# Kernel optimization log

Measured on AMD Instinct MI355X. Metric: run time of the kernel, lower is better.

The kernel has to match this reference:

```python
import jax, jax.numpy as jnp
import numpy as np

NUM_HEADS = 16
SPAN = 256  # pos_ebd_size (position_buckets)


def _split_heads(x, num_heads):
    # x: (B, S, D) -> (B*num_heads, S, D//num_heads)
    b, s, d = x.shape
    return x.reshape(b, s, num_heads, d // num_heads).transpose(0, 2, 1, 3).reshape(b * num_heads, s, d // num_heads)


def setup_inputs() -> dict:
    key = jax.random.key(0)
    ks = jax.random.split(key, 12)
    B, S, D = 1, 2048, 1024
    std = 0.02
    n_src = NUM_HEADS * S * 2 * SPAN   # flat size of c2p/p2c score tensor
    n_dst = NUM_HEADS * S * S          # flat size of gathered bias
    return {
        "hidden_states": jax.random.normal(ks[0], (B, S, D), jnp.float32),
        "rel_embeddings": jax.random.normal(ks[1], (2 * SPAN, D), jnp.float32),
        "Wq": jax.random.normal(ks[2], (D, D), jnp.float32) * std,
        "bq": jnp.zeros((D,), jnp.float32),
        "Wk": jax.random.normal(ks[3], (D, D), jnp.float32) * std,
        "bk": jnp.zeros((D,), jnp.float32),
        "Wv": jax.random.normal(ks[4], (D, D), jnp.float32) * std,
        "bv": jnp.zeros((D,), jnp.float32),
        "ids": jax.random.randint(ks[5], (n_dst,), 0, n_src, jnp.int32),
        "ids_t": jax.random.randint(ks[6], (n_dst,), 0, n_src, jnp.int32),
    }


def reference(hidden_states, rel_embeddings, Wq, bq, Wk, bk, Wv, bv, ids, ids_t):
    B, S, D = hidden_states.shape
    dh = D // NUM_HEADS
    # pos_att_type = ['c2p','p2c'] -> scale_factor = 3
    scale = jnp.sqrt(jnp.asarray(dh * 3, jnp.float32))

    q = _split_heads(hidden_states @ Wq + bq, NUM_HEADS)  # (B*H, S, dh)
    k = _split_heads(hidden_states @ Wk + bk, NUM_HEADS)
    v = _split_heads(hidden_states @ Wv + bv, NUM_HEADS)

    scores = jnp.einsum('bsd,btd->bst', q, k) / scale  # (B*H, S, S)

    # share_att_key=True: reuse key/query projections on relative embeddings
    pos = rel_embeddings[: 2 * SPAN][None]             # (1, 2*SPAN, D)
    pos_k = _split_heads(pos @ Wk + bk, NUM_HEADS)     # (H, 2*SPAN, dh)
    pos_q = _split_heads(pos @ Wq + bq, NUM_HEADS)

    bs = q.shape[0]  # == H when B == 1 (required by the original bmm)
    # c2p: gather from flattened (bs, S, 2*SPAN) scores
    c2p = jnp.einsum('bsd,bkd->bsk', q, pos_k)
    c2p_bias = c2p.reshape(-1)[ids].reshape(bs, S, S) / scale
    # p2c: gather then transpose last two dims
    p2c = jnp.einsum('bsd,bkd->bsk', k, pos_q)
    p2c_bias = jnp.swapaxes(p2c.reshape(-1)[ids_t].reshape(bs, S, S), -1, -2) / scale

    scores = scores + c2p_bias + p2c_bias
    probs = jax.nn.softmax(scores, axis=-1)
    ctx = jnp.einsum('bst,btd->bsd', probs, v)         # (B*H, S, dh)
    ctx = ctx.reshape(B, NUM_HEADS, S, dh).transpose(0, 2, 1, 3).reshape(B, S, D)
    return ctx
```

## Files before the change

kernel.cpp:

```cpp
#include <hip/hip_runtime.h>
#include <math.h>

#define S_LEN 2048
#define D_DIM 1024
#define NH 16
#define DH 64
#define NPOS 512
#define NT (S_LEN / 64)

typedef int   ivec4 __attribute__((ext_vector_type(4)));
typedef int   ivec2 __attribute__((ext_vector_type(2)));
typedef float fvec4 __attribute__((ext_vector_type(4)));

__device__ __forceinline__ void bar_lgkm() {
  asm volatile("s_waitcnt lgkmcnt(0)" ::: "memory");
  __builtin_amdgcn_s_barrier();
}

__global__ __launch_bounds__(256) void proj_gemm(
    const float* __restrict__ X, const float* __restrict__ W,
    const float* __restrict__ bias, float* __restrict__ outp, int M) {
  __shared__ float xt[16][132];
  __shared__ float wt[16][128];
  const int tid = threadIdx.x;
  const int br = blockIdx.y, bc = blockIdx.x;
  const int r0 = (tid >> 4) * 8, c0 = (tid & 15) * 8;
  float acc[8][8];
  #pragma unroll
  for (int i = 0; i < 8; i++)
    #pragma unroll
    for (int j = 0; j < 8; j++) acc[i][j] = 0.f;

  const float* Xb = X + (size_t)br * 128 * D_DIM;
  const float* Wb = W + bc * 128;

  for (int k0 = 0; k0 < D_DIM; k0 += 16) {
    __syncthreads();
    #pragma unroll
    for (int i = 0; i < 2; i++) {
      int slot = tid + i * 256;
      int row = slot >> 2;
      int kc = (slot & 3) * 4;
      float4 xv = *(const float4*)(Xb + (size_t)row * D_DIM + k0 + kc);
      xt[kc + 0][row] = xv.x; xt[kc + 1][row] = xv.y;
      xt[kc + 2][row] = xv.z; xt[kc + 3][row] = xv.w;
      int kr = slot >> 5;
      int wc = (slot & 31) * 4;
      *(float4*)&wt[kr][wc] = *(const float4*)(Wb + (size_t)(k0 + kr) * D_DIM + wc);
    }
    __syncthreads();
    #pragma unroll
    for (int kk = 0; kk < 16; kk++) {
      float a[8], b[8];
      *(float4*)&a[0] = *(const float4*)&xt[kk][r0];
      *(float4*)&a[4] = *(const float4*)&xt[kk][r0 + 4];
      *(float4*)&b[0] = *(const float4*)&wt[kk][c0];
      *(float4*)&b[4] = *(const float4*)&wt[kk][c0 + 4];
      #pragma unroll
      for (int ii = 0; ii < 8; ii++)
        #pragma unroll
        for (int jj = 0; jj < 8; jj++)
          acc[ii][jj] = fmaf(a[ii], b[jj], acc[ii][jj]);
    }
  }

  const int n0 = bc * 128 + c0;
  const int h = n0 >> 6, iw = n0 & 63;
  float bvals[8];
  #pragma unroll
  for (int jj = 0; jj < 8; jj++) bvals[jj] = bias[n0 + jj];
  #pragma unroll
  for (int ii = 0; ii < 8; ii++) {
    size_t row = (size_t)br * 128 + r0 + ii;
    float ov[8];
    #pragma unroll
    for (int jj = 0; jj < 8; jj++) ov[jj] = acc[ii][jj] + bvals[jj];
    float* dst = outp + ((size_t)h * M + row) * 64 + iw;
    *(float4*)dst = *(float4*)&ov[0];
    *(float4*)(dst + 4) = *(float4*)&ov[4];
  }
}

__global__ __launch_bounds__(256) void rel_gemm(
    const float* __restrict__ q_ws, const float* __restrict__ k_ws,
    const float* __restrict__ pk_ws, const float* __restrict__ pq_ws,
    float* __restrict__ c2p, float* __restrict__ p2c, float inv_scale) {
  __shared__ float at[16][132];
  __shared__ float bt[16][132];
  const int tid = threadIdx.x;
  const int h = blockIdx.z & 15;
  const int which = blockIdx.z >> 4;
  const float* A = (which ? k_ws : q_ws) + (size_t)h * S_LEN * DH;
  const float* Bm = (which ? pq_ws : pk_ws) + (size_t)h * NPOS * DH;
  float* C = (which ? p2c : c2p) + (size_t)h * S_LEN * NPOS;
  const int br = blockIdx.y, bc = blockIdx.x;
  const int r0 = (tid >> 4) * 8, c0 = (tid & 15) * 8;
  float acc[8][8];
  #pragma unroll
  for (int i = 0; i < 8; i++)
    #pragma unroll
    for (int j = 0; j < 8; j++) acc[i][j] = 0.f;

  for (int k0 = 0; k0 < DH; k0 += 16) {
    __syncthreads();
    #pragma unroll
    for (int i = 0; i < 2; i++) {
      int slot = tid + i * 256;
      int row = slot >> 2;
      int kc = (slot & 3) * 4;
      float4 av = *(const float4*)(A + (size_t)(br * 128 + row) * DH + k0 + kc);
      at[kc + 0][row] = av.x; at[kc + 1][row] = av.y;
      at[kc + 2][row] = av.z; at[kc + 3][row] = av.w;
      float4 bv = *(const float4*)(Bm + (size_t)(bc * 128 + row) * DH + k0 + kc);
      bt[kc + 0][row] = bv.x; bt[kc + 1][row] = bv.y;
      bt[kc + 2][row] = bv.z; bt[kc + 3][row] = bv.w;
    }
    __syncthreads();
    #pragma unroll
    for (int kk = 0; kk < 16; kk++) {
      float a[8], b[8];
      *(float4*)&a[0] = *(const float4*)&at[kk][r0];
      *(float4*)&a[4] = *(const float4*)&at[kk][r0 + 4];
      *(float4*)&b[0] = *(const float4*)&bt[kk][c0];
      *(float4*)&b[4] = *(const float4*)&bt[kk][c0 + 4];
      #pragma unroll
      for (int ii = 0; ii < 8; ii++)
        #pragma unroll
        for (int jj = 0; jj < 8; jj++)
          acc[ii][jj] = fmaf(a[ii], b[jj], acc[ii][jj]);
    }
  }
  #pragma unroll
  for (int ii = 0; ii < 8; ii++) {
    size_t row = (size_t)br * 128 + r0 + ii;
    float ov[8];
    #pragma unroll
    for (int jj = 0; jj < 8; jj++) ov[jj] = acc[ii][jj] * inv_scale;
    float* dst = C + row * NPOS + bc * 128 + c0;
    *(float4*)dst = *(float4*)&ov[0];
    *(float4*)(dst + 4) = *(float4*)&ov[4];
  }
}

__global__ __launch_bounds__(512, 4) void attn_kernel(
    const float* __restrict__ q_ws, const float* __restrict__ k_ws,
    const float* __restrict__ v_ws, const float* __restrict__ c2p,
    const float* __restrict__ p2c, const int* __restrict__ ids,
    const int* __restrict__ ids_t, float* __restrict__ outp, float inv_scale) {
  __shared__ float qT[64][68];
  __shared__ float kT[64][68];
  __shared__ float vS[64][64];
  const int tid = threadIdx.x;
  const int h = blockIdx.y;
  const int s0 = blockIdx.x * 64;
  const int r4 = tid >> 4;
  const int c4 = tid & 15;
  const int r0 = r4 * 2;
  const int c0 = c4 * 4;

  const float* qb = q_ws + ((size_t)h * S_LEN + s0) * DH;
  const float* kb = k_ws + (size_t)h * S_LEN * DH;
  const float* vb = v_ws + (size_t)h * S_LEN * DH;
  const int* idc = ids   + (size_t)h * S_LEN * S_LEN;
  const int* idp = ids_t + (size_t)h * S_LEN * S_LEN;

  #pragma unroll
  for (int i = 0; i < 2; i++) {
    int slot = tid + i * 512;
    int s = slot >> 4;
    int dc = (slot & 15) * 4;
    float4 qv = *(const float4*)(qb + (size_t)s * DH + dc);
    qT[dc + 0][s] = qv.x; qT[dc + 1][s] = qv.y;
    qT[dc + 2][s] = qv.z; qT[dc + 3][s] = qv.w;
  }

  float m[2], l[2], o[2][4];
  #pragma unroll
  for (int ii = 0; ii < 2; ii++) {
    m[ii] = -INFINITY; l[ii] = 0.f;
    #pragma unroll
    for (int jj = 0; jj < 4; jj++) o[ii][jj] = 0.f;
  }

  ivec4 ia[2];
  ivec2 ib[4];
  #pragma unroll
  for (int ii = 0; ii < 2; ii++)
    ia[ii] = __builtin_nontemporal_load(
        (const ivec4*)(idc + (size_t)(s0 + r0 + ii) * S_LEN + c0));
  #pragma unroll
  for (int jj = 0; jj < 4; jj++)
    ib[jj] = __builtin_nontemporal_load(
        (const ivec2*)(idp + (size_t)(c0 + jj) * S_LEN + s0 + r0));

  for (int kt = 0; kt < NT; kt++) {
    const int t0 = kt * 64;

    float4 kreg[2], vreg[2];
    int ts[2], dcs[2];
    #pragma unroll
    for (int i = 0; i < 2; i++) {
      int slot = tid + i * 512;
      ts[i] = slot >> 4;
      dcs[i] = (slot & 15) * 4;
      kreg[i] = *(const float4*)(kb + (size_t)(t0 + ts[i]) * DH + dcs[i]);
      vreg[i] = *(const float4*)(vb + (size_t)(t0 + ts[i]) * DH + dcs[i]);
    }

    float gc[2][4], gp[4][2];
    #pragma unroll
    for (int ii = 0; ii < 2; ii++) {
      gc[ii][0] = c2p[ia[ii][0]]; gc[ii][1] = c2p[ia[ii][1]];
      gc[ii][2] = c2p[ia[ii][2]]; gc[ii][3] = c2p[ia[ii][3]];
    }
    #pragma unroll
    for (int jj = 0; jj < 4; jj++) {
      gp[jj][0] = p2c[ib[jj][0]];
      gp[jj][1] = p2c[ib[jj][1]];
    }

    bar_lgkm();
    #pragma unroll
    for (int i = 0; i < 2; i++) {
      kT[dcs[i] + 0][ts[i]] = kreg[i].x; kT[dcs[i] + 1][ts[i]] = kreg[i].y;
      kT[dcs[i] + 2][ts[i]] = kreg[i].z; kT[dcs[i] + 3][ts[i]] = kreg[i].w;
      *(float4*)&vS[ts[i]][dcs[i]] = vreg[i];
    }
    bar_lgkm();

    float sc[2][4];
    #pragma unroll
    for (int ii = 0; ii < 2; ii++)
      #pragma unroll
      for (int jj = 0; jj < 4; jj++) sc[ii][jj] = 0.f;
    #pragma unroll 8
    for (int d = 0; d < 64; d++) {
      float a[2], b[4];
      *(float2*)a = *(const float2*)&qT[d][r0];
      *(float4*)b = *(const float4*)&kT[d][c0];
      #pragma unroll
      for (int ii = 0; ii < 2; ii++)
        #pragma unroll
        for (int jj = 0; jj < 4; jj++)
          sc[ii][jj] = fmaf(a[ii], b[jj], sc[ii][jj]);
    }

    if (kt + 1 < NT) {
      #pragma unroll
      for (int ii = 0; ii < 2; ii++)
        ia[ii] = __builtin_nontemporal_load(
            (const ivec4*)(idc + (size_t)(s0 + r0 + ii) * S_LEN + t0 + 64 + c0));
      #pragma unroll
      for (int jj = 0; jj < 4; jj++)
        ib[jj] = __builtin_nontemporal_load(
            (const ivec2*)(idp + (size_t)(t0 + 64 + c0 + jj) * S_LEN + s0 + r0));
    }

    #pragma unroll
    for (int ii = 0; ii < 2; ii++)
      #pragma unroll
      for (int jj = 0; jj < 4; jj++)
        sc[ii][jj] = fmaf(sc[ii][jj], inv_scale, gc[ii][jj] + gp[jj][ii]);

    #pragma unroll
    for (int ii = 0; ii < 2; ii++) {
      float v = fmaxf(fmaxf(sc[ii][0], sc[ii][1]), fmaxf(sc[ii][2], sc[ii][3]));
      v = fmaxf(v, __shfl_xor(v, 1));
      v = fmaxf(v, __shfl_xor(v, 2));
      v = fmaxf(v, __shfl_xor(v, 4));
      v = fmaxf(v, __shfl_xor(v, 8));
      float mn = fmaxf(m[ii], v);
      float alpha = __expf(m[ii] - mn);
      m[ii] = mn;
      float rs = 0.f;
      #pragma unroll
      for (int jj = 0; jj < 4; jj++) {
        sc[ii][jj] = __expf(sc[ii][jj] - mn);
        rs += sc[ii][jj];
      }
      rs += __shfl_xor(rs, 1);
      rs += __shfl_xor(rs, 2);
      rs += __shfl_xor(rs, 4);
      rs += __shfl_xor(rs, 8);
      l[ii] = l[ii] * alpha + rs;
      #pragma unroll
      for (int jj = 0; jj < 4; jj++) o[ii][jj] *= alpha;
    }

    bar_lgkm();
    #pragma unroll
    for (int jj = 0; jj < 4; jj++) {
      float pv[2] = {sc[0][jj], sc[1][jj]};
      *(float2*)&kT[c0 + jj][r0] = *(float2*)pv;
    }
    bar_lgkm();

    #pragma unroll 8
    for (int t = 0; t < 64; t++) {
      float a[2], b[4];
      *(float2*)a = *(const float2*)&kT[t][r0];
      *(float4*)b = *(const float4*)&vS[t][c0];
      #pragma unroll
      for (int ii = 0; ii < 2; ii++)
        #pragma unroll
        for (int jj = 0; jj < 4; jj++)
          o[ii][jj] = fmaf(a[ii], b[jj], o[ii][jj]);
    }
  }

  #pragma unroll
  for (int ii = 0; ii < 2; ii++) {
    float inv_l = 1.0f / l[ii];
    fvec4 ov;
    #pragma unroll
    for (int jj = 0; jj < 4; jj++) ov[jj] = o[ii][jj] * inv_l;
    float* dst = outp + (size_t)(s0 + r0 + ii) * D_DIM + h * DH + c0;
    __builtin_nontemporal_store(ov, (fvec4*)dst);
  }
}

extern "C" void kernel_launch(void* const* d_in, const int* in_sizes, int n_in,
                              void* d_out, int out_size, void* d_ws, size_t ws_size,
                              hipStream_t stream) {
  const float* hs  = (const float*)d_in[0];
  const float* rel = (const float*)d_in[1];
  const float* Wq  = (const float*)d_in[2];
  const float* bq  = (const float*)d_in[3];
  const float* Wk  = (const float*)d_in[4];
  const float* bk  = (const float*)d_in[5];
  const float* Wv  = (const float*)d_in[6];
  const float* bv  = (const float*)d_in[7];
  const int* ids   = (const int*)d_in[8];
  const int* ids_t = (const int*)d_in[9];
  float* outp = (float*)d_out;

  float* ws = (float*)d_ws;
  float* q_ws  = ws;
  float* k_ws  = q_ws + 2097152;
  float* v_ws  = k_ws + 2097152;
  float* pk_ws = v_ws + 2097152;
  float* pq_ws = pk_ws + 524288;
  float* c2p_ws = pq_ws + 524288;
  float* p2c_ws = c2p_ws + 16777216;

  const float inv_scale = 1.0f / sqrtf((float)(DH * 3));

  dim3 blk(256);
  proj_gemm<<<dim3(8, 16), blk, 0, stream>>>(hs, Wq, bq, q_ws, S_LEN);
  proj_gemm<<<dim3(8, 16), blk, 0, stream>>>(hs, Wk, bk, k_ws, S_LEN);
  proj_gemm<<<dim3(8, 16), blk, 0, stream>>>(hs, Wv, bv, v_ws, S_LEN);
  proj_gemm<<<dim3(8, 4),  blk, 0, stream>>>(rel, Wk, bk, pk_ws, NPOS);
  proj_gemm<<<dim3(8, 4),  blk, 0, stream>>>(rel, Wq, bq, pq_ws, NPOS);
  rel_gemm<<<dim3(4, 16, 32), blk, 0, stream>>>(q_ws, k_ws, pk_ws, pq_ws,
                                                c2p_ws, p2c_ws, inv_scale);
  attn_kernel<<<dim3(32, 16), dim3(512), 0, stream>>>(
      q_ws, k_ws, v_ws, c2p_ws, p2c_ws, ids, ids_t, outp, inv_scale);
}
```

Baseline: 3.605 ms.

## Merge five projection GEMMs into one launch with double-buffered LDS prefetch

The five separate projection GEMM launches are replaced by one kernel that selects its operands from blockIdx.z, so the small rel-embedding projections share the device with the large ones and launch overhead drops. The k-loop now uses double-buffered shared memory and issues the next tile's global loads into registers before computing on the current tile, hiding load latency. It doubles LDS use and raises register pressure, and blocks with no rows early-exit in the z=3,4 slices.

```diff
diff --git a/kernel.cpp b/kernel.cpp
--- a/kernel.cpp
+++ b/kernel.cpp
@@ -17,13 +17,29 @@
   __builtin_amdgcn_s_barrier();
 }
 
-__global__ __launch_bounds__(256) void proj_gemm(
-    const float* __restrict__ X, const float* __restrict__ W,
-    const float* __restrict__ bias, float* __restrict__ outp, int M) {
-  __shared__ float xt[16][132];
-  __shared__ float wt[16][128];
+__global__ __launch_bounds__(256) void proj_gemm5(
+    const float* __restrict__ hs, const float* __restrict__ rel,
+    const float* __restrict__ Wq, const float* __restrict__ bq,
+    const float* __restrict__ Wk, const float* __restrict__ bk,
+    const float* __restrict__ Wv, const float* __restrict__ bv,
+    float* __restrict__ q_ws, float* __restrict__ k_ws,
+    float* __restrict__ v_ws, float* __restrict__ pk_ws,
+    float* __restrict__ pq_ws) {
+  const int z = blockIdx.z;
+  const float* X; const float* W; const float* bias; float* outp; int M;
+  switch (z) {
+    case 0:  X = hs;  W = Wq; bias = bq; outp = q_ws;  M = S_LEN; break;
+    case 1:  X = hs;  W = Wk; bias = bk; outp = k_ws;  M = S_LEN; break;
+    case 2:  X = hs;  W = Wv; bias = bv; outp = v_ws;  M = S_LEN; break;
+    case 3:  X = rel; W = Wk; bias = bk; outp = pk_ws; M = NPOS;  break;
+    default: X = rel; W = Wq; bias = bq; outp = pq_ws; M = NPOS;  break;
+  }
+  const int br = blockIdx.y, bc = blockIdx.x;
+  if (br * 128 >= M) return;
+
+  __shared__ float xt[2][16][132];
+  __shared__ float wt[2][16][128];
   const int tid = threadIdx.x;
-  const int br = blockIdx.y, bc = blockIdx.x;
   const int r0 = (tid >> 4) * 8, c0 = (tid & 15) * 8;
   float acc[8][8];
   #pragma unroll
@@ -34,34 +50,55 @@
   const float* Xb = X + (size_t)br * 128 * D_DIM;
   const float* Wb = W + bc * 128;
 
+  int row_[2], kc_[2], kr_[2], wc_[2];
+  #pragma unroll
+  for (int i = 0; i < 2; i++) {
+    int slot = tid + i * 256;
+    row_[i] = slot >> 2;
+    kc_[i] = (slot & 3) * 4;
+    kr_[i] = slot >> 5;
+    wc_[i] = (slot & 31) * 4;
+  }
+
+  float4 xv[2], wv[2];
+  #pragma unroll
+  for (int i = 0; i < 2; i++) {
+    xv[i] = *(const float4*)(Xb + (size_t)row_[i] * D_DIM + kc_[i]);
+    wv[i] = *(const float4*)(Wb + (size_t)kr_[i] * D_DIM + wc_[i]);
+  }
+
   for (int k0 = 0; k0 < D_DIM; k0 += 16) {
-    __syncthreads();
+    const int buf = (k0 >> 4) & 1;
     #pragma unroll
     for (int i = 0; i < 2; i++) {
-      int slot = tid + i * 256;
-      int row = slot >> 2;
-      int kc = (slot & 3) * 4;
-      float4 xv = *(const float4*)(Xb + (size_t)row * D_DIM + k0 + kc);
-      xt[kc + 0][row] = xv.x; xt[kc + 1][row] = xv.y;
-      xt[kc + 2][row] = xv.z; xt[kc + 3][row] = xv.w;
-      int kr = slot >> 5;
-      int wc = (slot & 31) * 4;
-      *(float4*)&wt[kr][wc] = *(const float4*)(Wb + (size_t)(k0 + kr) * D_DIM + wc);
-    }
-    __syncthreads();
+      xt[buf][kc_[i] + 0][row_[i]] = xv[i].x;
+      xt[buf][kc_[i] + 1][row_[i]] = xv[i].y;
+      xt[buf][kc_[i] + 2][row_[i]] = xv[i].z;
+      xt[buf][kc_[i] + 3][row_[i]] = xv[i].w;
+      *(float4*)&wt[buf][kr_[i]][wc_[i]] = wv[i];
+    }
+    bar_lgkm();
+    if (k0 + 16 < D_DIM) {
+      #pragma unroll
+      for (int i = 0; i < 2; i++) {
+        xv[i] = *(const float4*)(Xb + (size_t)row_[i] * D_DIM + k0 + 16 + kc_[i]);
+        wv[i] = *(const float4*)(Wb + (size_t)(k0 + 16 + kr_[i]) * D_DIM + wc_[i]);
+      }
+    }
     #pragma unroll
     for (int kk = 0; kk < 16; kk++) {
       float a[8], b[8];
-      *(float4*)&a[0] = *(const float4*)&xt[kk][r0];
-      *(float4*)&a[4] = *(const float4*)&xt[kk][r0 + 4];
-      *(float4*)&b[0] = *(const float4*)&wt[kk][c0];
-      *(float4*)&b[4] = *(const float4*)&wt[kk][c0 + 4];
+      *(float4*)&a[0] = *(const float4*)&xt[buf][kk][r0];
+      *(float4*)&a[4] = *(const float4*)&xt[buf][kk][r0 + 4];
+      *(float4*)&b[0] = *(const float4*)&wt[buf][kk][c0];
+      *(float4*)&b[4] = *(const float4*)&wt[buf][kk][c0 + 4];
       #pragma unroll
       for (int ii = 0; ii < 8; ii++)
         #pragma unroll
         for (int jj = 0; jj < 8; jj++)
           acc[ii][jj] = fmaf(a[ii], b[jj], acc[ii][jj]);
     }
+    bar_lgkm();
   }
 
   const int n0 = bc * 128 + c0;
@@ -345,14 +382,10 @@
 
   const float inv_scale = 1.0f / sqrtf((float)(DH * 3));
 
-  dim3 blk(256);
-  proj_gemm<<<dim3(8, 16), blk, 0, stream>>>(hs, Wq, bq, q_ws, S_LEN);
-  proj_gemm<<<dim3(8, 16), blk, 0, stream>>>(hs, Wk, bk, k_ws, S_LEN);
-  proj_gemm<<<dim3(8, 16), blk, 0, stream>>>(hs, Wv, bv, v_ws, S_LEN);
-  proj_gemm<<<dim3(8, 4),  blk, 0, stream>>>(rel, Wk, bk, pk_ws, NPOS);
-  proj_gemm<<<dim3(8, 4),  blk, 0, stream>>>(rel, Wq, bq, pq_ws, NPOS);
-  rel_gemm<<<dim3(4, 16, 32), blk, 0, stream>>>(q_ws, k_ws, pk_ws, pq_ws,
-                                                c2p_ws, p2c_ws, inv_scale);
+  proj_gemm5<<<dim3(8, 16, 5), dim3(256), 0, stream>>>(
+      hs, rel, Wq, bq, Wk, bk, Wv, bv, q_ws, k_ws, v_ws, pk_ws, pq_ws);
+  rel_gemm<<<dim3(4, 16, 32), dim3(256), 0, stream>>>(
+      q_ws, k_ws, pk_ws, pq_ws, c2p_ws, p2c_ws, inv_scale);
   attn_kernel<<<dim3(32, 16), dim3(512), 0, stream>>>(
       q_ws, k_ws, v_ws, c2p_ws, p2c_ws, ids, ids_t, outp, inv_scale);
 }
```

New measurement: 3.163 ms. -12.3%, faster.
